# Kernel optimization log

Measured on AMD Instinct MI355X. Metric: run time of the kernel, lower is better.

The kernel has to match this reference:

```python
import jax, jax.numpy as jnp
import numpy as np
from jax import lax

B, L, DM = 1, 2048, 1024   # batch, seq len, d_model
N = 16                     # d_state
K = 4                      # d_conv
DI = 2 * DM                # d_inner = d_model * expand_factor


def silu(v):
    return v * jax.nn.sigmoid(v)


def setup_inputs() -> dict:
    key = jax.random.key(0)
    ks = jax.random.split(key, 11)
    s = 0.02
    f32 = jnp.float32
    return {
        "x": jax.random.normal(ks[0], (B, L, DM), f32),
        "W_in": jax.random.normal(ks[1], (2 * DI, DM), f32) * s,
        "b_in": jnp.zeros((2 * DI,), f32),
        "W_conv": jax.random.normal(ks[2], (DI, 1, K), f32) * s,  # depthwise conv kernel (torch layout)
        "b_conv": jnp.zeros((DI,), f32),
        "W_x": jax.random.normal(ks[3], (DI + 2 * N, DI), f32) * s,
        "b_x": jnp.zeros((DI + 2 * N,), f32),
        "W_out": jax.random.normal(ks[4], (DM, DI), f32) * s,
        "b_out": jnp.zeros((DM,), f32),
        "A_log": jax.random.normal(ks[5], (DI, N), f32),
        "D": jnp.ones((DI,), f32),
    }


def reference(x, W_in, b_in, W_conv, b_conv, W_x, b_x, W_out, b_out, A_log, D):
    Bsz = x.shape[0]
    # in_proj and split into ssm branch / residual gate branch
    xr = x @ W_in.T + b_in                      # (B, L, 2*DI)
    xi, res = jnp.split(xr, 2, axis=-1)
    # causal depthwise conv1d: torch pads (K-1) both sides then slices [:L] == left-pad K-1
    xc = jnp.transpose(xi, (0, 2, 1))           # (B, DI, L)
    xc = lax.conv_general_dilated(
        xc, W_conv, window_strides=(1,), padding=[(K - 1, 0)],
        dimension_numbers=("NCH", "OIH", "NCH"), feature_group_count=DI,
    ) + b_conv[None, :, None]
    xi = silu(jnp.transpose(xc, (0, 2, 1)))     # (B, L, DI)
    # selective-scan parameterization
    proj = xi @ W_x.T + b_x                      # (B, L, DI + 2N)
    delta = jax.nn.softplus(proj[..., :DI])      # (B, L, DI)
    B_ssm = proj[..., DI:DI + N]                 # (B, L, N)
    C_ssm = proj[..., DI + N:]                   # (B, L, N)
    A = -jnp.exp(A_log)                          # (DI, N)
    dA = jnp.exp(delta[..., None] * A)                               # (B, L, DI, N)
    dBx = delta[..., None] * B_ssm[:, :, None, :] * xi[..., None]    # (B, L, DI, N)

    def step(h, inp):
        da, dbx, c = inp
        h = da * h + dbx                         # (B, DI, N)
        y = jnp.einsum("bdn,bn->bd", h, c)
        return h, y

    h0 = jnp.zeros((Bsz, DI, N), x.dtype)
    _, ys = lax.scan(
        step, h0,
        (jnp.swapaxes(dA, 0, 1), jnp.swapaxes(dBx, 0, 1), jnp.swapaxes(C_ssm, 0, 1)),
    )
    y = jnp.swapaxes(ys, 0, 1) + xi * D          # skip connection
    y = y * silu(res)                            # gate
    return y @ W_out.T + b_out                   # (B, L, DM)
```

## Files before the change

kernel.cpp:

```cpp
#include <hip/hip_runtime.h>
#include <stdint.h>

#define L_SEQ 2048
#define DMODEL 1024
#define DI_DIM 2048
#define NSSM 16
#define NPROJ 2080
#define NCHUNK 64
#define LCHUNK 32

typedef __attribute__((ext_vector_type(8))) short bf16x8;
typedef __attribute__((ext_vector_type(4))) float f32x4;

__device__ __forceinline__ float bf2f(unsigned short u) {
  union { uint32_t u; float f; } v; v.u = (uint32_t)u << 16; return v.f;
}
__device__ __forceinline__ unsigned short f2bf(float f) {
  union { float f; uint32_t u; } v; v.f = f;
  uint32_t u = v.u;
  return (unsigned short)((u + 0x7fffu + ((u >> 16) & 1u)) >> 16);
}
__device__ __forceinline__ void async16(const void* g, void* l) {
  __builtin_amdgcn_global_load_lds(
      (__attribute__((address_space(1))) void*)(g),
      (__attribute__((address_space(3))) void*)(l), 16, 0, 0);
}
__device__ __forceinline__ float softplusf(float p) {
  return (p > 20.f) ? p : __logf(1.f + __expf(p));
}
__device__ __forceinline__ float siluf(float x) {
  return x * __builtin_amdgcn_rcpf(1.f + __expf(-x));
}

#define CVT_N1 524288
#define CVT_N2 (CVT_N1 + 1048576)
#define CVT_N3 (CVT_N2 + 1064960)
__global__ void k_convert3(const float* __restrict__ x, const float* __restrict__ win,
                           const float* __restrict__ wx, unsigned short* __restrict__ xb,
                           unsigned short* __restrict__ winb, unsigned short* __restrict__ wxb) {
  int i = blockIdx.x * 256 + threadIdx.x;
  const float4* src; unsigned short* dst; int j;
  if (i < CVT_N1)      { src = (const float4*)x;   dst = xb;   j = i; }
  else if (i < CVT_N2) { src = (const float4*)win; dst = winb; j = i - CVT_N1; }
  else if (i < CVT_N3) { src = (const float4*)wx;  dst = wxb;  j = i - CVT_N2; }
  else return;
  float4 v = src[j];
  ushort4 o;
  o.x = f2bf(v.x); o.y = f2bf(v.y); o.z = f2bf(v.z); o.w = f2bf(v.w);
  ((ushort4*)dst)[j] = o;
}

__global__ void k_f32_to_bf16(const float* __restrict__ in,
                              unsigned short* __restrict__ out, int n4) {
  int i = blockIdx.x * blockDim.x + threadIdx.x;
  if (i < n4) {
    const float4 v = ((const float4*)in)[i];
    ushort4 o;
    o.x = f2bf(v.x); o.y = f2bf(v.y); o.z = f2bf(v.z); o.w = f2bf(v.w);
    ((ushort4*)out)[i] = o;
  }
}

template <typename OutT>
__global__ __launch_bounds__(256) void k_gemm_bt(
    const unsigned short* __restrict__ A, const unsigned short* __restrict__ B,
    const float* __restrict__ bias, OutT* __restrict__ C,
    int M, int N, int K) {
  __shared__ unsigned short As[2][64 * 32];
  __shared__ unsigned short Bs[2][128 * 32];
  const int tid = threadIdx.x;
  const int wave = tid >> 6;
  const int lane = tid & 63;
  const int m0 = blockIdx.y * 64;
  const int n0 = blockIdx.x * 128;
  const int kLen = K / gridDim.z;
  const int kLo = blockIdx.z * kLen;

  const int scol = (lane & 3) * 8;
  int ar = m0 + wave * 16 + (lane >> 2);       if (ar > M - 1) ar = M - 1;
  int br0 = n0 + wave * 32 + (lane >> 2);      if (br0 > N - 1) br0 = N - 1;
  int br1 = n0 + wave * 32 + 16 + (lane >> 2); if (br1 > N - 1) br1 = N - 1;
  const unsigned short* ap  = A + (size_t)ar * K + scol + kLo;
  const unsigned short* bp0 = B + (size_t)br0 * K + scol + kLo;
  const unsigned short* bp1 = B + (size_t)br1 * K + scol + kLo;
  const int soA  = (wave * 16) * 32;
  const int soB0 = (wave * 32) * 32;
  const int soB1 = (wave * 32 + 16) * 32;

  const int fr = lane & 15;
  const int fk = (lane >> 4) * 8;

  f32x4 acc[4][2];
#pragma unroll
  for (int i = 0; i < 4; i++)
#pragma unroll
    for (int j = 0; j < 2; j++) acc[i][j] = (f32x4){0.f, 0.f, 0.f, 0.f};

  const int niter = kLen / 32;

  async16(ap, &As[0][soA]);
  async16(bp0, &Bs[0][soB0]);
  async16(bp1, &Bs[0][soB1]);

#define GEMM_COMPUTE(BUF)                                                      \
  {                                                                            \
    bf16x8 af[4], bfv[2];                                                      \
    _Pragma("unroll")                                                          \
    for (int i = 0; i < 4; i++)                                                \
      af[i] = *(const bf16x8*)&As[BUF][(i * 16 + fr) * 32 + fk];               \
    _Pragma("unroll")                                                          \
    for (int j = 0; j < 2; j++)                                                \
      bfv[j] = *(const bf16x8*)&Bs[BUF][(wave * 32 + j * 16 + fr) * 32 + fk];  \
    _Pragma("unroll")                                                          \
    for (int i = 0; i < 4; i++)                                                \
      _Pragma("unroll")                                                        \
      for (int j = 0; j < 2; j++)                                              \
        acc[i][j] = __builtin_amdgcn_mfma_f32_16x16x32_bf16(af[i], bfv[j],     \
                                                            acc[i][j], 0, 0, 0); \
  }

  for (int it = 0; it < niter; it += 2) {
    __syncthreads();
    {
      int kt = (it + 1) * 32;
      async16(ap + kt, &As[1][soA]);
      async16(bp0 + kt, &Bs[1][soB0]);
      async16(bp1 + kt, &Bs[1][soB1]);
    }
    GEMM_COMPUTE(0)
    __syncthreads();
    if (it + 2 < niter) {
      int kt = (it + 2) * 32;
      async16(ap + kt, &As[0][soA]);
      async16(bp0 + kt, &Bs[0][soB0]);
      async16(bp1 + kt, &Bs[0][soB1]);
    }
    GEMM_COMPUTE(1)
  }
#undef GEMM_COMPUTE

  const bool withBias = (gridDim.z == 1);
  OutT* Cz = C + (size_t)blockIdx.z * ((size_t)M * N);
#pragma unroll
  for (int j = 0; j < 2; j++) {
    int col = n0 + wave * 32 + j * 16 + fr;
    if (col < N) {
      float bv = withBias ? bias[col] : 0.f;
#pragma unroll
      for (int i = 0; i < 4; i++) {
        int rbase = m0 + i * 16 + (lane >> 4) * 4;
#pragma unroll
        for (int r = 0; r < 4; r++) {
          float v = acc[i][j][r] + bv;
          if constexpr (sizeof(OutT) == 2)
            Cz[(size_t)(rbase + r) * N + col] = (OutT)f2bf(v);
          else
            Cz[(size_t)(rbase + r) * N + col] = (OutT)v;
        }
      }
    }
  }
}

__global__ void k_reduce_out(const float* __restrict__ part, const float* __restrict__ bias,
                             float* __restrict__ out) {
  int i = blockIdx.x * 256 + threadIdx.x;
  float4 a = ((const float4*)part)[i];
  float4 b = ((const float4*)(part + (size_t)L_SEQ * DMODEL))[i];
  int col = (i * 4) & (DMODEL - 1);
  float4 bb = *(const float4*)&bias[col];
  float4 o;
  o.x = a.x + b.x + bb.x; o.y = a.y + b.y + bb.y;
  o.z = a.z + b.z + bb.z; o.w = a.w + b.w + bb.w;
  ((float4*)out)[i] = o;
}

__global__ void k_conv_silu(const unsigned short* __restrict__ xr,
                            const float* __restrict__ Wc,
                            const float* __restrict__ bc,
                            unsigned short* __restrict__ xcb) {
  int idx = blockIdx.x * blockDim.x + threadIdx.x;
  if (idx >= L_SEQ * DI_DIM) return;
  int t = idx >> 11;
  int d = idx & (DI_DIM - 1);
  float acc = bc[d];
  const float* wd = Wc + d * 4;
  if (t >= 3) acc += bf2f(xr[(size_t)(t - 3) * (2 * DI_DIM) + d]) * wd[0];
  if (t >= 2) acc += bf2f(xr[(size_t)(t - 2) * (2 * DI_DIM) + d]) * wd[1];
  if (t >= 1) acc += bf2f(xr[(size_t)(t - 1) * (2 * DI_DIM) + d]) * wd[2];
  acc += bf2f(xr[(size_t)t * (2 * DI_DIM) + d]) * wd[3];
  xcb[idx] = f2bf(siluf(acc));
}

__global__ __launch_bounds__(256) void k_scan_a(
    const float* __restrict__ proj, const unsigned short* __restrict__ xcb,
    const float* __restrict__ A_log,
    float* __restrict__ Sdelta, float* __restrict__ hstate) {
  __shared__ float Bsh[LCHUNK * NSSM];
  const int d = blockIdx.x * 256 + threadIdx.x;
  const int c = blockIdx.y;
  const int t0 = c * LCHUNK;
  for (int i = threadIdx.x; i < LCHUNK * NSSM; i += 256) {
    int t = i >> 4, n = i & 15;
    Bsh[i] = proj[(size_t)(t0 + t) * NPROJ + DI_DIM + n];
  }
  __syncthreads();
  float Ar[NSSM], h[NSSM];
#pragma unroll
  for (int n = 0; n < NSSM; n++) {
    Ar[n] = -__expf(A_log[d * NSSM + n]);
    h[n] = 0.f;
  }
  const float* pp = proj + (size_t)t0 * NPROJ + d;
  const unsigned short* xp = xcb + (size_t)t0 * DI_DIM + d;
  float p_nxt = pp[0];
  unsigned short x_nxt = xp[0];
  float sd = 0.f;
  for (int t = 0; t < LCHUNK; t++) {
    float p = p_nxt;
    unsigned short xu = x_nxt;
    if (t + 1 < LCHUNK) {
      p_nxt = pp[(size_t)(t + 1) * NPROJ];
      x_nxt = xp[(size_t)(t + 1) * DI_DIM];
    }
    float delta = softplusf(p);
    float dx = delta * bf2f(xu);
    sd += delta;
#pragma unroll
    for (int n = 0; n < NSSM; n++)
      h[n] = __expf(delta * Ar[n]) * h[n] + dx * Bsh[t * NSSM + n];
  }
  Sdelta[(size_t)c * DI_DIM + d] = sd;
#pragma unroll
  for (int n = 0; n < NSSM; n++)
    hstate[((size_t)c * DI_DIM + d) * NSSM + n] = h[n];
}

__global__ void k_scan_b(const float* __restrict__ A_log,
                         const float* __restrict__ Sdelta,
                         float* __restrict__ hstate) {
  int tid = blockIdx.x * 256 + threadIdx.x;
  int d = tid >> 4;
  float A = -__expf(A_log[tid]);
  float carry = 0.f;
  float v_nxt = hstate[tid];
  float s_nxt = Sdelta[d];
  for (int c = 0; c < NCHUNK; c++) {
    float v = v_nxt, s = s_nxt;
    if (c + 1 < NCHUNK) {
      v_nxt = hstate[(size_t)(c + 1) * DI_DIM * NSSM + tid];
      s_nxt = Sdelta[(size_t)(c + 1) * DI_DIM + d];
    }
    hstate[(size_t)c * DI_DIM * NSSM + tid] = carry;
    carry = __expf(A * s) * carry + v;
  }
}

__global__ __launch_bounds__(256) void k_scan_c(
    const float* __restrict__ proj, const unsigned short* __restrict__ xcb,
    const float* __restrict__ A_log, const float* __restrict__ h0,
    const float* __restrict__ Dvec, const unsigned short* __restrict__ xr,
    unsigned short* __restrict__ ybf) {
  __shared__ float Bsh[LCHUNK * NSSM];
  __shared__ float Csh[LCHUNK * NSSM];
  const int d = blockIdx.x * 256 + threadIdx.x;
  const int c = blockIdx.y;
  const int t0 = c * LCHUNK;
  for (int i = threadIdx.x; i < LCHUNK * NSSM; i += 256) {
    int t = i >> 4, n = i & 15;
    Bsh[i] = proj[(size_t)(t0 + t) * NPROJ + DI_DIM + n];
    Csh[i] = proj[(size_t)(t0 + t) * NPROJ + DI_DIM + NSSM + n];
  }
  __syncthreads();
  float Ar[NSSM], h[NSSM];
#pragma unroll
  for (int n = 0; n < NSSM; n++) {
    Ar[n] = -__expf(A_log[d * NSSM + n]);
    h[n] = h0[((size_t)c * DI_DIM + d) * NSSM + n];
  }
  float Dd = Dvec[d];
  const float* pp = proj + (size_t)t0 * NPROJ + d;
  const unsigned short* xp = xcb + (size_t)t0 * DI_DIM + d;
  const unsigned short* rp = xr + (size_t)t0 * (2 * DI_DIM) + DI_DIM + d;
  float p_nxt = pp[0];
  unsigned short x_nxt = xp[0];
  unsigned short r_nxt = rp[0];
  for (int t = 0; t < LCHUNK; t++) {
    float p = p_nxt;
    unsigned short xu = x_nxt, ru = r_nxt;
    if (t + 1 < LCHUNK) {
      p_nxt = pp[(size_t)(t + 1) * NPROJ];
      x_nxt = xp[(size_t)(t + 1) * DI_DIM];
      r_nxt = rp[(size_t)(t + 1) * (2 * DI_DIM)];
    }
    float delta = softplusf(p);
    float xi = bf2f(xu);
    float dx = delta * xi;
    float y = 0.f;
#pragma unroll
    for (int n = 0; n < NSSM; n++) {
      h[n] = __expf(delta * Ar[n]) * h[n] + dx * Bsh[t * NSSM + n];
      y += h[n] * Csh[t * NSSM + n];
    }
    y += xi * Dd;
    y *= siluf(bf2f(ru));
    ybf[(size_t)(t0 + t) * DI_DIM + d] = f2bf(y);
  }
}

extern "C" void kernel_launch(void* const* d_in, const int* in_sizes, int n_in,
                              void* d_out, int out_size, void* d_ws, size_t ws_size,
                              hipStream_t stream) {
  const float* x      = (const float*)d_in[0];
  const float* W_in   = (const float*)d_in[1];
  const float* b_in   = (const float*)d_in[2];
  const float* W_conv = (const float*)d_in[3];
  const float* b_conv = (const float*)d_in[4];
  const float* W_x    = (const float*)d_in[5];
  const float* b_x    = (const float*)d_in[6];
  const float* W_out  = (const float*)d_in[7];
  const float* b_out  = (const float*)d_in[8];
  const float* A_log  = (const float*)d_in[9];
  const float* Dv     = (const float*)d_in[10];
  float* out = (float*)d_out;

  char* ws = (char*)d_ws;
  size_t off = 0;
  auto alloc = [&](size_t bytes) { void* p = ws + off; off += (bytes + 255) & ~(size_t)255; return p; };
  unsigned short* win_bf = (unsigned short*)alloc((size_t)4096 * DMODEL * 2);
  unsigned short* wx_bf  = (unsigned short*)alloc((size_t)NPROJ * DI_DIM * 2);
  unsigned short* x_bf   = (unsigned short*)alloc((size_t)L_SEQ * DMODEL * 2);
  unsigned short* xr_bf  = (unsigned short*)alloc((size_t)L_SEQ * 2 * DI_DIM * 2);
  unsigned short* xcb    = (unsigned short*)alloc((size_t)L_SEQ * DI_DIM * 2);
  float* proj            = (float*)alloc((size_t)L_SEQ * NPROJ * 4);
  float* Sdelta          = (float*)alloc((size_t)NCHUNK * DI_DIM * 4);
  float* hstate          = (float*)alloc((size_t)NCHUNK * DI_DIM * NSSM * 4);
  if (off > ws_size) return;
  unsigned short* ybf     = win_bf;
  unsigned short* wout_bf = x_bf;
  float* part             = proj;

  k_convert3<<<CVT_N3 / 256, 256, 0, stream>>>(x, W_in, W_x, x_bf, win_bf, wx_bf);

  {
    dim3 g(4096 / 128, L_SEQ / 64);
    k_gemm_bt<unsigned short><<<g, 256, 0, stream>>>(x_bf, win_bf, b_in, xr_bf, L_SEQ, 4096, DMODEL);
  }
  k_f32_to_bf16<<<(DMODEL * DI_DIM / 4) / 256, 256, 0, stream>>>(W_out, wout_bf, DMODEL * DI_DIM / 4);
  k_conv_silu<<<(L_SEQ * DI_DIM) / 256, 256, 0, stream>>>(xr_bf, W_conv, b_conv, xcb);
  {
    dim3 g((NPROJ + 127) / 128, L_SEQ / 64);
    k_gemm_bt<float><<<g, 256, 0, stream>>>(xcb, wx_bf, b_x, proj, L_SEQ, NPROJ, DI_DIM);
  }
  {
    dim3 ga(DI_DIM / 256, NCHUNK);
    k_scan_a<<<ga, 256, 0, stream>>>(proj, xcb, A_log, Sdelta, hstate);
    k_scan_b<<<(DI_DIM * NSSM) / 256, 256, 0, stream>>>(A_log, Sdelta, hstate);
    k_scan_c<<<ga, 256, 0, stream>>>(proj, xcb, A_log, hstate, Dv, xr_bf, ybf);
  }
  {
    dim3 g(DMODEL / 128, L_SEQ / 64, 2);
    k_gemm_bt<float><<<g, 256, 0, stream>>>(ybf, wout_bf, b_out, part, L_SEQ, DMODEL, DI_DIM);
    k_reduce_out<<<(L_SEQ * DMODEL / 4) / 256, 256, 0, stream>>>(part, b_out, out);
  }
}
```

Baseline: 281.0 us.

## Triple-buffer GEMM LDS with BK=64 and vmcnt-based async wait

Restructures the bf16 GEMM main loop from a double buffer with K-step 32 to a three-stage ring buffer with K-step 64. Two tiles stay in flight, and s_waitcnt vmcnt(6) plus a raw s_barrier replace __syncthreads, so the next stage's loads overlap compute with half as many barriers per K. The cost is roughly three times the LDS footprint (72KB), which can lower occupancy. The code also assumes niter is at least 2 and relies on vmcnt accounting being correct for the async LDS loads.

After: 289.5 us. 3.0% more time.

```diff
diff --git a/kernel.cpp b/kernel.cpp
--- a/kernel.cpp
+++ b/kernel.cpp
@@ -66,8 +66,8 @@
     const unsigned short* __restrict__ A, const unsigned short* __restrict__ B,
     const float* __restrict__ bias, OutT* __restrict__ C,
     int M, int N, int K) {
-  __shared__ unsigned short As[2][64 * 32];
-  __shared__ unsigned short Bs[2][128 * 32];
+  __shared__ unsigned short As[3][64 * 64];
+  __shared__ unsigned short Bs[3][128 * 64];
   const int tid = threadIdx.x;
   const int wave = tid >> 6;
   const int lane = tid & 63;
@@ -96,47 +96,59 @@
 #pragma unroll
     for (int j = 0; j < 2; j++) acc[i][j] = (f32x4){0.f, 0.f, 0.f, 0.f};
 
-  const int niter = kLen / 32;
-
-  async16(ap, &As[0][soA]);
-  async16(bp0, &Bs[0][soB0]);
-  async16(bp1, &Bs[0][soB1]);
+  const int niter = kLen / 64;
+
+#define STAGE(BUF, KT)                                                         \
+  {                                                                            \
+    unsigned short* As_ = &As[BUF][0];                                         \
+    unsigned short* Bs_ = &Bs[BUF][0];                                         \
+    async16(ap + (KT),       As_ + soA);                                       \
+    async16(ap + (KT) + 32,  As_ + 2048 + soA);                                \
+    async16(bp0 + (KT),      Bs_ + soB0);                                      \
+    async16(bp0 + (KT) + 32, Bs_ + 4096 + soB0);                               \
+    async16(bp1 + (KT),      Bs_ + soB1);                                      \
+    async16(bp1 + (KT) + 32, Bs_ + 4096 + soB1);                               \
+  }
 
 #define GEMM_COMPUTE(BUF)                                                      \
   {                                                                            \
-    bf16x8 af[4], bfv[2];                                                      \
     _Pragma("unroll")                                                          \
-    for (int i = 0; i < 4; i++)                                                \
-      af[i] = *(const bf16x8*)&As[BUF][(i * 16 + fr) * 32 + fk];               \
-    _Pragma("unroll")                                                          \
-    for (int j = 0; j < 2; j++)                                                \
-      bfv[j] = *(const bf16x8*)&Bs[BUF][(wave * 32 + j * 16 + fr) * 32 + fk];  \
-    _Pragma("unroll")                                                          \
-    for (int i = 0; i < 4; i++)                                                \
+    for (int kk = 0; kk < 2; kk++) {                                           \
+      bf16x8 af[4], bfv[2];                                                    \
+      _Pragma("unroll")                                                        \
+      for (int i = 0; i < 4; i++)                                              \
+        af[i] = *(const bf16x8*)&As[BUF][kk * 2048 + (i * 16 + fr) * 32 + fk]; \
       _Pragma("unroll")                                                        \
       for (int j = 0; j < 2; j++)                                              \
-        acc[i][j] = __builtin_amdgcn_mfma_f32_16x16x32_bf16(af[i], bfv[j],     \
-                                                            acc[i][j], 0, 0, 0); \
-  }
-
-  for (int it = 0; it < niter; it += 2) {
-    __syncthreads();
-    {
-      int kt = (it + 1) * 32;
-      async16(ap + kt, &As[1][soA]);
-      async16(bp0 + kt, &Bs[1][soB0]);
-      async16(bp1 + kt, &Bs[1][soB1]);
-    }
-    GEMM_COMPUTE(0)
-    __syncthreads();
+        bfv[j] = *(const bf16x8*)&Bs[BUF][kk * 4096 +                          \
+                                          (wave * 32 + j * 16 + fr) * 32 + fk];\
+      _Pragma("unroll")                                                        \
+      for (int i = 0; i < 4; i++)                                              \
+        _Pragma("unroll")                                                      \
+        for (int j = 0; j < 2; j++)                                            \
+          acc[i][j] = __builtin_amdgcn_mfma_f32_16x16x32_bf16(af[i], bfv[j],   \
+                                                          acc[i][j], 0, 0, 0); \
+    }                                                                          \
+  }
+
+  STAGE(0, 0)
+  STAGE(1, 64)
+
+  int rb = 0;
+  for (int it = 0; it < niter - 1; ++it) {
+    asm volatile("s_waitcnt vmcnt(6)" ::: "memory");
+    asm volatile("s_barrier" ::: "memory");
     if (it + 2 < niter) {
-      int kt = (it + 2) * 32;
-      async16(ap + kt, &As[0][soA]);
-      async16(bp0 + kt, &Bs[0][soB0]);
-      async16(bp1 + kt, &Bs[0][soB1]);
-    }
-    GEMM_COMPUTE(1)
-  }
+      int wb = rb + 2; if (wb >= 3) wb -= 3;
+      STAGE(wb, (it + 2) * 64)
+    }
+    GEMM_COMPUTE(rb)
+    rb = (rb == 2) ? 0 : rb + 1;
+  }
+  asm volatile("s_waitcnt vmcnt(0)" ::: "memory");
+  asm volatile("s_barrier" ::: "memory");
+  GEMM_COMPUTE(rb)
+#undef STAGE
 #undef GEMM_COMPUTE
 
   const bool withBias = (gridDim.z == 1);
```
